# Kernel tuning notes

Hardware: AMD Instinct MI355X
Metric: run time of the kernel (lower is better)

## Reference

```python
import jax, jax.numpy as jnp
import numpy as np

K = 3        # kernel_size
STRIDE = 1
PAD = 1
DIL = 1


def setup_inputs() -> dict:
    key = jax.random.key(0)
    ks = jax.random.split(key, 5)
    B, C, H, W, O = 4, 64, 128, 128, 64
    x = jax.random.normal(ks[0], (B, C, H, W), jnp.float32)
    # small offset-conv weights -> offsets of a few pixels (realistic trained regime)
    offset_w = jax.random.normal(ks[1], (2 * K * K, C, K, K), jnp.float32) * 0.01
    offset_b = jax.random.normal(ks[2], (2 * K * K,), jnp.float32) * 0.01
    weight = jax.random.normal(ks[3], (O, C, K, K), jnp.float32)
    bias = jax.random.normal(ks[4], (O,), jnp.float32)
    return {"x": x, "offset_w": offset_w, "offset_b": offset_b,
            "weight": weight, "bias": bias}


def _conv2d(x, w, b):
    y = jax.lax.conv_general_dilated(
        x, w, window_strides=(STRIDE, STRIDE),
        padding=[(PAD, PAD), (PAD, PAD)],
        dimension_numbers=("NCHW", "OIHW", "NCHW"))
    return y + b[None, :, None, None]


def _deform_conv2d(x, offset, weight, bias):
    B, C, H, W = x.shape
    O = weight.shape[0]
    KK = K * K
    Ho, Wo = offset.shape[2], offset.shape[3]
    # offset channels ordered (y, x) per kernel tap: [B, KK, 2, Ho, Wo]
    off = offset.reshape(B, KK, 2, Ho, Wo)
    kyy, kxx = jnp.meshgrid(jnp.arange(K) * DIL, jnp.arange(K) * DIL, indexing="ij")
    kyy = kyy.reshape(KK).astype(x.dtype)
    kxx = kxx.reshape(KK).astype(x.dtype)
    base_y = (jnp.arange(Ho) * STRIDE - PAD).astype(x.dtype)
    base_x = (jnp.arange(Wo) * STRIDE - PAD).astype(x.dtype)
    # sampling positions [B, KK, Ho, Wo]
    py = base_y[None, None, :, None] + kyy[None, :, None, None] + off[:, :, 0]
    px = base_x[None, None, None, :] + kxx[None, :, None, None] + off[:, :, 1]

    y0 = jnp.floor(py); x0 = jnp.floor(px)
    y1 = y0 + 1.0;      x1 = x0 + 1.0
    wy1 = py - y0; wy0 = 1.0 - wy1
    wx1 = px - x0; wx0 = 1.0 - wx1

    xf = x.reshape(B, C, H * W)

    def corner(yc, xc):
        valid = (yc >= 0) & (yc < H) & (xc >= 0) & (xc < W)  # zero padding outside
        idx = (jnp.clip(yc, 0, H - 1) * W + jnp.clip(xc, 0, W - 1)).astype(jnp.int32)
        g = jax.vmap(lambda xb, ib: xb[:, ib.reshape(-1)])(xf, idx)  # [B, C, KK*Ho*Wo]
        g = g.reshape(B, C, KK, Ho, Wo)
        return g * valid[:, None].astype(x.dtype)

    val = (corner(y0, x0) * (wy0 * wx0)[:, None]
         + corner(y0, x1) * (wy0 * wx1)[:, None]
         + corner(y1, x0) * (wy1 * wx0)[:, None]
         + corner(y1, x1) * (wy1 * wx1)[:, None])  # [B, C, KK, Ho, Wo]

    out = jnp.einsum("bckhw,ock->bohw", val, weight.reshape(O, C, KK))
    return out + bias[None, :, None, None]


def reference(x, offset_w, offset_b, weight, bias):
    offset = _conv2d(x, offset_w, offset_b)
    return _deform_conv2d(x, offset, weight, bias)
```

## Files before the change

### kernel.cpp

```cpp
#include <hip/hip_runtime.h>

#define B_   4
#define C_   64
#define O_   64
#define H_   128
#define W_   128
#define HW_  (H_ * W_)
#define KK_  9
#define M_   18

typedef short  short8  __attribute__((ext_vector_type(8)));
typedef float  floatx4 __attribute__((ext_vector_type(4)));
typedef unsigned short ushort4v __attribute__((ext_vector_type(4)));
typedef unsigned short ushort8v __attribute__((ext_vector_type(8)));

static __device__ __forceinline__ unsigned short f2bf(float f) {
    unsigned int u = __float_as_uint(f);
    u += 0x7FFFu + ((u >> 16) & 1u);
    return (unsigned short)(u >> 16);
}
static __device__ __forceinline__ float bf2f(unsigned short s) {
    return __uint_as_float((unsigned int)s << 16);
}

__global__ __launch_bounds__(256) void prep(
        const float* __restrict__ x, const float* __restrict__ w,
        const float* __restrict__ ow, unsigned short* __restrict__ xT,
        unsigned short* __restrict__ wtbf, unsigned short* __restrict__ owtbf) {
    const int blk = blockIdx.x;
    if (blk < 512) {
        __shared__ unsigned short T[128][72];
        const int tid = threadIdx.x;
        const int y = blk & (H_ - 1);
        const int b = blk >> 7;
        const float* xby = x + (size_t)b * C_ * HW_ + y * W_;
        for (int i = tid; i < C_ * W_; i += 256) {
            const int c = i >> 7, xc = i & 127;
            T[xc][c] = f2bf(xby[(size_t)c * HW_ + xc]);
        }
        __syncthreads();
        unsigned short* dst = xT + (size_t)b * (4 * HW_ * 16) + y * (W_ * 16);
        for (int j = tid; j < 2048; j += 256) {
            const int g  = j >> 9;
            const int x8 = (j >> 2) & 127;
            const int c0 = (j & 3) * 4;
            const ushort4v pk = *(const ushort4v*)&T[x8][g * 16 + c0];
            *(ushort4v*)&dst[(size_t)g * (HW_ * 16) + x8 * 16 + c0] = pk;
        }
    } else if (blk < 530) {
        const int i = (blk - 512) * 256 + threadIdx.x;
        const int lane = i & 63, rest = i >> 6;
        const int ot = rest & 3, cks = rest >> 2;
        const int chunk = cks / 6, ks = cks % 6;
        const int o = ot * 16 + (lane & 15);
        const int kbase = chunk * 192 + ks * 32 + (lane >> 4) * 8;
        ushort8v pk;
        #pragma unroll
        for (int j = 0; j < 8; ++j) {
            const int k = kbase + j;
            pk[j] = f2bf(w[o * 576 + (k & 63) * 9 + (k >> 6)]);
        }
        *(ushort8v*)&wtbf[(size_t)i * 8] = pk;
    } else {
        const int i = (blk - 530) * 256 + threadIdx.x;
        const int lane = i & 63, rest = i >> 6;
        const int tile = rest & 1, tks = rest >> 1;
        const int tap = tks >> 1, ks = tks & 1;
        const int m = tile * 16 + (lane & 15);
        const int cb = ks * 32 + (lane >> 4) * 8;
        ushort8v pk;
        #pragma unroll
        for (int j = 0; j < 8; ++j)
            pk[j] = (m < M_) ? f2bf(ow[m * 576 + (cb + j) * 9 + tap])
                             : (unsigned short)0;
        *(ushort8v*)&owtbf[(size_t)i * 8] = pk;
    }
}

__global__ __launch_bounds__(256, 4) void dcn_fused(
        const unsigned short* __restrict__ xT,
        const unsigned short* __restrict__ owtbf, const float* __restrict__ ob,
        const unsigned short* __restrict__ wtbf, const float* __restrict__ bias,
        float* __restrict__ out) {
    __shared__ union {
        unsigned short P[3][66][72];
        float ep[4][64][17];
    } u;
    __shared__ float offs[4][M_][16];

    const int tid    = threadIdx.x;
    const int lane   = tid & 63;
    const int wslot  = __builtin_amdgcn_readfirstlane(tid >> 6);
    const int lane15 = lane & 15;
    const int quad   = lane >> 4;

    const int g    = blockIdx.x;
    const int xcd  = g & 7;
    const int slot = g >> 3;
    const int ho   = xcd * 16 + (slot >> 3);
    const int b    = (slot >> 1) & 3;
    const int wo_base = (slot & 1) << 6;

    const unsigned short* xTb = xT + (size_t)b * (4 * HW_ * 16);

    #pragma unroll
    for (int it = 0; it < 3; ++it) {
        const int t  = it * 4 + wslot;
        const int ky = t >> 2, cgp = t & 3;
        const int y  = ho - 1 + ky;
        const bool yv = (unsigned)y < (unsigned)H_;
        const unsigned short* src = xTb + (size_t)cgp * (HW_ * 16) + y * (W_ * 16);
        #pragma unroll
        for (int pass = 0; pass < 2; ++pass) {
            const int r = pass * 64 + lane;
            if (r < 66) {
                const int cx = wo_base + r - 1;
                ushort8v p0 = {0, 0, 0, 0, 0, 0, 0, 0};
                ushort8v p1 = {0, 0, 0, 0, 0, 0, 0, 0};
                if (yv && (unsigned)cx < (unsigned)W_) {
                    p0 = *(const ushort8v*)&src[cx * 16];
                    p1 = *(const ushort8v*)&src[cx * 16 + 8];
                }
                *(ushort8v*)&u.P[ky][r][cgp * 16]     = p0;
                *(ushort8v*)&u.P[ky][r][cgp * 16 + 8] = p1;
            }
        }
    }
    __syncthreads();

    floatx4 oa0 = (floatx4){0.f, 0.f, 0.f, 0.f};
    floatx4 oa1 = (floatx4){0.f, 0.f, 0.f, 0.f};
    {
        const int pxt = wslot;
        #pragma unroll
        for (int ky = 0; ky < 3; ++ky) {
            #pragma unroll
            for (int kx = 0; kx < 3; ++kx) {
                const int tap = ky * 3 + kx;
                #pragma unroll
                for (int ks = 0; ks < 2; ++ks) {
                    const int kk = ks * 32 + quad * 8;
                    const short8 af =
                        *(const short8*)&u.P[ky][pxt * 16 + lane15 + kx][kk];
                    const int fb = ((tap * 2 + ks) * 2) * 64 + lane;
                    const short8 bf0 = *(const short8*)&owtbf[(size_t)fb * 8];
                    const short8 bf1 =
                        *(const short8*)&owtbf[(size_t)(fb + 64) * 8];
                    oa0 = __builtin_amdgcn_mfma_f32_16x16x32_bf16(af, bf0, oa0, 0, 0, 0);
                    oa1 = __builtin_amdgcn_mfma_f32_16x16x32_bf16(af, bf1, oa1, 0, 0, 0);
                }
            }
        }
    }
    {
        const float ob0 = ob[lane15];
        #pragma unroll
        for (int r = 0; r < 4; ++r) oa0[r] += ob0;
        *(floatx4*)&offs[wslot][lane15][quad * 4] = oa0;
        if (lane15 < 2) {
            const float ob1 = ob[16 + lane15];
            #pragma unroll
            for (int r = 0; r < 4; ++r) oa1[r] += ob1;
            *(floatx4*)&offs[wslot][16 + lane15][quad * 4] = oa1;
        }
    }
    __syncthreads();

    const int p   = wslot;
    const int pxg = p * 16 + lane15;
    floatx4 acc[4];
    #pragma unroll
    for (int t = 0; t < 4; ++t) acc[t] = (floatx4){0.f, 0.f, 0.f, 0.f};

    for (int chunk = 0; chunk < 3; ++chunk) {
        #pragma unroll
        for (int tl = 0; tl < 3; ++tl) {
            const int k  = chunk * 3 + tl;
            const int ky = k / 3, kx = k % 3;
            const float offy = offs[wslot][2 * k][lane15];
            const float offx = offs[wslot][2 * k + 1][lane15];
            const float py  = (float)(ho - 1 + ky) + offy;
            const float pxx = (float)(wo_base - 1 + kx + pxg) + offx;
            const float fy = floorf(py), fx = floorf(pxx);
            const int y0 = (int)fy, x0 = (int)fx;
            const int y1 = y0 + 1,  x1 = x0 + 1;
            const float wy1 = py - fy,  wy0 = 1.f - wy1;
            const float wx1 = pxx - fx, wx0 = 1.f - wx1;
            const bool y0v = (unsigned)y0 < (unsigned)H_;
            const bool y1v = (unsigned)y1 < (unsigned)H_;
            const bool x0v = (unsigned)x0 < (unsigned)W_;
            const bool x1v = (unsigned)x1 < (unsigned)W_;
            const float w00 = (y0v && x0v) ? wy0 * wx0 : 0.f;
            const float w01 = (y0v && x1v) ? wy0 * wx1 : 0.f;
            const float w10 = (y1v && x0v) ? wy1 * wx0 : 0.f;
            const float w11 = (y1v && x1v) ? wy1 * wx1 : 0.f;
            const int ry0 = min(max(y0, 0), H_ - 1);
            const int ry1 = min(max(y1, 0), H_ - 1);
            const int cx0 = min(max(x0, 0), W_ - 1);
            const int cx1 = min(max(x1, 0), W_ - 1);
            const int a00 = (ry0 * W_ + cx0) * 16;
            const int a01 = (ry0 * W_ + cx1) * 16;
            const int a10 = (ry1 * W_ + cx0) * 16;
            const int a11 = (ry1 * W_ + cx1) * 16;
            #pragma unroll
            for (int chalf = 0; chalf < 2; ++chalf) {
                const int c0 = chalf * 32 + quad * 8;
                const unsigned short* xp =
                    xTb + (size_t)(c0 >> 4) * (HW_ * 16) + (c0 & 8);
                const ushort8v q00 = *(const ushort8v*)&xp[a00];
                const ushort8v q01 = *(const ushort8v*)&xp[a01];
                const ushort8v q10 = *(const ushort8v*)&xp[a10];
                const ushort8v q11 = *(const ushort8v*)&xp[a11];
                ushort8v pk;
                #pragma unroll
                for (int j = 0; j < 8; ++j)
                    pk[j] = f2bf(bf2f(q00[j]) * w00 + bf2f(q01[j]) * w01
                               + bf2f(q10[j]) * w10 + bf2f(q11[j]) * w11);
                const short8 af = *(const short8*)&pk;
                const int cks = chunk * 6 + tl * 2 + chalf;
                #pragma unroll
                for (int t = 0; t < 4; ++t) {
                    const short8 bfrag = *(const short8*)
                        &wtbf[(size_t)((cks * 4 + t) * 64 + lane) * 8];
                    acc[t] = __builtin_amdgcn_mfma_f32_16x16x32_bf16(
                                 af, bfrag, acc[t], 0, 0, 0);
                }
            }
        }
    }

    float* epw = &u.ep[wslot][0][0];
    #pragma unroll
    for (int t = 0; t < 4; ++t)
        #pragma unroll
        for (int r = 0; r < 4; ++r)
            epw[(t * 16 + lane15) * 17 + quad * 4 + r] = acc[t][r];

    const int wo = wo_base + p * 16 + lane15;
    #pragma unroll
    for (int i = 0; i < 16; ++i) {
        const int o = i * 4 + quad;
        out[(size_t)(b * O_ + o) * HW_ + ho * W_ + wo] =
            epw[o * 17 + lane15] + bias[o];
    }
}

extern "C" void kernel_launch(void* const* d_in, const int* in_sizes, int n_in,
                              void* d_out, int out_size, void* d_ws, size_t ws_size,
                              hipStream_t stream) {
    const float* x    = (const float*)d_in[0];
    const float* ow   = (const float*)d_in[1];
    const float* ob   = (const float*)d_in[2];
    const float* w    = (const float*)d_in[3];
    const float* bias = (const float*)d_in[4];
    float* out = (float*)d_out;

    unsigned short* wtbf  = (unsigned short*)d_ws;
    unsigned short* owtbf = wtbf + 4608 * 8;
    unsigned short* xT    = owtbf + 2304 * 8;

    prep<<<539, 256, 0, stream>>>(x, w, ow, xT, wtbf, owtbf);
    dcn_fused<<<B_ * H_ * (W_ / 64), 256, 0, stream>>>(xT, owtbf, ob, wtbf, bias, out);
}
```

Measured before the change: 110.7 us.

## Switch to single-wave 32-pixel blocks using 32x32x16 MFMA

Restructures the fused deformable conv kernel so that each block is a single 64-thread wavefront covering 32 output pixels. Both the offset conv and the main GEMM now use 32x32x16 bf16 MFMAs, and the weight prep layouts are repacked to match. The shared-memory input staging tile and the __syncthreads barriers are removed; the offset conv reads xT directly from global memory. This reduces LDS traffic and synchronization and doubles the number of blocks, at the cost of more global loads for the offset conv and less intra-block reuse.

```diff
diff --git a/kernel.cpp b/kernel.cpp
--- a/kernel.cpp
+++ b/kernel.cpp
@@ -9,8 +9,8 @@
 #define KK_  9
 #define M_   18
 
-typedef short  short8  __attribute__((ext_vector_type(8)));
-typedef float  floatx4 __attribute__((ext_vector_type(4)));
+typedef short  short8   __attribute__((ext_vector_type(8)));
+typedef float  floatx16 __attribute__((ext_vector_type(16)));
 typedef unsigned short ushort4v __attribute__((ext_vector_type(4)));
 typedef unsigned short ushort8v __attribute__((ext_vector_type(8)));
 
@@ -22,6 +22,8 @@
 static __device__ __forceinline__ float bf2f(unsigned short s) {
     return __uint_as_float((unsigned int)s << 16);
 }
+
+#define ZERO16 {0.f,0.f,0.f,0.f,0.f,0.f,0.f,0.f,0.f,0.f,0.f,0.f,0.f,0.f,0.f,0.f}
 
 __global__ __launch_bounds__(256) void prep(
         const float* __restrict__ x, const float* __restrict__ w,
@@ -50,24 +52,22 @@
     } else if (blk < 530) {
         const int i = (blk - 512) * 256 + threadIdx.x;
         const int lane = i & 63, rest = i >> 6;
-        const int ot = rest & 3, cks = rest >> 2;
-        const int chunk = cks / 6, ks = cks % 6;
-        const int o = ot * 16 + (lane & 15);
-        const int kbase = chunk * 192 + ks * 32 + (lane >> 4) * 8;
+        const int t = rest & 1, s = rest >> 1;
+        const int o  = t * 32 + (lane & 31);
+        const int kb = s * 16 + (lane >> 5) * 8;
         ushort8v pk;
         #pragma unroll
         for (int j = 0; j < 8; ++j) {
-            const int k = kbase + j;
+            const int k = kb + j;
             pk[j] = f2bf(w[o * 576 + (k & 63) * 9 + (k >> 6)]);
         }
         *(ushort8v*)&wtbf[(size_t)i * 8] = pk;
     } else {
         const int i = (blk - 530) * 256 + threadIdx.x;
-        const int lane = i & 63, rest = i >> 6;
-        const int tile = rest & 1, tks = rest >> 1;
-        const int tap = tks >> 1, ks = tks & 1;
-        const int m = tile * 16 + (lane & 15);
-        const int cb = ks * 32 + (lane >> 4) * 8;
+        const int lane = i & 63, s = i >> 6;
+        const int m   = lane & 31;
+        const int tap = s >> 2;
+        const int cb  = (s & 3) * 16 + (lane >> 5) * 8;
         ushort8v pk;
         #pragma unroll
         for (int j = 0; j < 8; ++j)
@@ -77,171 +77,121 @@
     }
 }
 
-__global__ __launch_bounds__(256, 4) void dcn_fused(
+__global__ __launch_bounds__(64, 4) void dcn_fused(
         const unsigned short* __restrict__ xT,
         const unsigned short* __restrict__ owtbf, const float* __restrict__ ob,
         const unsigned short* __restrict__ wtbf, const float* __restrict__ bias,
         float* __restrict__ out) {
-    __shared__ union {
-        unsigned short P[3][66][72];
-        float ep[4][64][17];
-    } u;
-    __shared__ float offs[4][M_][16];
-
-    const int tid    = threadIdx.x;
-    const int lane   = tid & 63;
-    const int wslot  = __builtin_amdgcn_readfirstlane(tid >> 6);
-    const int lane15 = lane & 15;
-    const int quad   = lane >> 4;
+    __shared__ float offs[M_][33];
+    __shared__ float epw[64][33];
+
+    const int lane = threadIdx.x;
+    const int pxl  = lane & 31;
+    const int kh   = lane >> 5;
+    const int khOff = kh * 8;
 
     const int g    = blockIdx.x;
     const int xcd  = g & 7;
     const int slot = g >> 3;
-    const int ho   = xcd * 16 + (slot >> 3);
-    const int b    = (slot >> 1) & 3;
-    const int wo_base = (slot & 1) << 6;
+    const int ho   = xcd * 16 + (slot >> 4);
+    const int rest = slot & 15;
+    const int b    = rest >> 2;
+    const int wo_base = (rest & 3) << 5;
 
     const unsigned short* xTb = xT + (size_t)b * (4 * HW_ * 16);
 
+    floatx16 oa = ZERO16;
+    for (int tap = 0; tap < 9; ++tap) {
+        const int ky = tap / 3, kx = tap % 3;
+        const int y    = ho - 1 + ky;
+        const int xcol = wo_base - 1 + kx + pxl;
+        const bool valid = ((unsigned)y < (unsigned)H_) &&
+                           ((unsigned)xcol < (unsigned)W_);
+        const int yc = min(max(y, 0), H_ - 1);
+        const int xc = min(max(xcol, 0), W_ - 1);
+        const int base = (yc * W_ + xc) * 16 + khOff;
+        #pragma unroll
+        for (int sl = 0; sl < 4; ++sl) {
+            ushort8v q = {0, 0, 0, 0, 0, 0, 0, 0};
+            if (valid)
+                q = *(const ushort8v*)&xTb[(size_t)sl * (HW_ * 16) + base];
+            const short8 af = *(const short8*)&q;
+            const int s = tap * 4 + sl;
+            const short8 bf = *(const short8*)&owtbf[(size_t)(s * 64 + lane) * 8];
+            oa = __builtin_amdgcn_mfma_f32_32x32x16_bf16(af, bf, oa, 0, 0, 0);
+        }
+    }
+    if (pxl < M_) {
+        const float obm = ob[pxl];
+        #pragma unroll
+        for (int r = 0; r < 16; ++r) {
+            const int px = (r & 3) + 8 * (r >> 2) + 4 * kh;
+            offs[pxl][px] = oa[r] + obm;
+        }
+    }
+
+    floatx16 acc0 = ZERO16, acc1 = ZERO16;
+    for (int tap = 0; tap < 9; ++tap) {
+        const int ky = tap / 3, kx = tap % 3;
+        const float offy = offs[2 * tap][pxl];
+        const float offx = offs[2 * tap + 1][pxl];
+        const float py  = (float)(ho - 1 + ky) + offy;
+        const float pxx = (float)(wo_base - 1 + kx + pxl) + offx;
+        const float fy = floorf(py), fx = floorf(pxx);
+        const int y0 = (int)fy, x0 = (int)fx;
+        const int y1 = y0 + 1,  x1 = x0 + 1;
+        const float wy1 = py - fy,  wy0 = 1.f - wy1;
+        const float wx1 = pxx - fx, wx0 = 1.f - wx1;
+        const bool y0v = (unsigned)y0 < (unsigned)H_;
+        const bool y1v = (unsigned)y1 < (unsigned)H_;
+        const bool x0v = (unsigned)x0 < (unsigned)W_;
+        const bool x1v = (unsigned)x1 < (unsigned)W_;
+        const float w00 = (y0v && x0v) ? wy0 * wx0 : 0.f;
+        const float w01 = (y0v && x1v) ? wy0 * wx1 : 0.f;
+        const float w10 = (y1v && x0v) ? wy1 * wx0 : 0.f;
+        const float w11 = (y1v && x1v) ? wy1 * wx1 : 0.f;
+        const int ry0 = min(max(y0, 0), H_ - 1);
+        const int ry1 = min(max(y1, 0), H_ - 1);
+        const int cx0 = min(max(x0, 0), W_ - 1);
+        const int cx1 = min(max(x1, 0), W_ - 1);
+        const int a00 = (ry0 * W_ + cx0) * 16 + khOff;
+        const int a01 = (ry0 * W_ + cx1) * 16 + khOff;
+        const int a10 = (ry1 * W_ + cx0) * 16 + khOff;
+        const int a11 = (ry1 * W_ + cx1) * 16 + khOff;
+        #pragma unroll
+        for (int sl = 0; sl < 4; ++sl) {
+            const unsigned short* xp = xTb + (size_t)sl * (HW_ * 16);
+            const ushort8v q00 = *(const ushort8v*)&xp[a00];
+            const ushort8v q01 = *(const ushort8v*)&xp[a01];
+            const ushort8v q10 = *(const ushort8v*)&xp[a10];
+            const ushort8v q11 = *(const ushort8v*)&xp[a11];
+            ushort8v pk;
+            #pragma unroll
+            for (int j = 0; j < 8; ++j)
+                pk[j] = f2bf(bf2f(q00[j]) * w00 + bf2f(q01[j]) * w01
+                           + bf2f(q10[j]) * w10 + bf2f(q11[j]) * w11);
+            const short8 af = *(const short8*)&pk;
+            const int s = tap * 4 + sl;
+            const short8 bf0 = *(const short8*)
+                &wtbf[(size_t)((s * 2 + 0) * 64 + lane) * 8];
+            const short8 bf1 = *(const short8*)
+                &wtbf[(size_t)((s * 2 + 1) * 64 + lane) * 8];
+            acc0 = __builtin_amdgcn_mfma_f32_32x32x16_bf16(af, bf0, acc0, 0, 0, 0);
+            acc1 = __builtin_amdgcn_mfma_f32_32x32x16_bf16(af, bf1, acc1, 0, 0, 0);
+        }
+    }
+
     #pragma unroll
-    for (int it = 0; it < 3; ++it) {
-        const int t  = it * 4 + wslot;
-        const int ky = t >> 2, cgp = t & 3;
-        const int y  = ho - 1 + ky;
-        const bool yv = (unsigned)y < (unsigned)H_;
-        const unsigned short* src = xTb + (size_t)cgp * (HW_ * 16) + y * (W_ * 16);
-        #pragma unroll
-        for (int pass = 0; pass < 2; ++pass) {
-            const int r = pass * 64 + lane;
-            if (r < 66) {
-                const int cx = wo_base + r - 1;
-                ushort8v p0 = {0, 0, 0, 0, 0, 0, 0, 0};
-                ushort8v p1 = {0, 0, 0, 0, 0, 0, 0, 0};
-                if (yv && (unsigned)cx < (unsigned)W_) {
-                    p0 = *(const ushort8v*)&src[cx * 16];
-                    p1 = *(const ushort8v*)&src[cx * 16 + 8];
-                }
-                *(ushort8v*)&u.P[ky][r][cgp * 16]     = p0;
-                *(ushort8v*)&u.P[ky][r][cgp * 16 + 8] = p1;
-            }
-        }
-    }
-    __syncthreads();
-
-    floatx4 oa0 = (floatx4){0.f, 0.f, 0.f, 0.f};
-    floatx4 oa1 = (floatx4){0.f, 0.f, 0.f, 0.f};
-    {
-        const int pxt = wslot;
-        #pragma unroll
-        for (int ky = 0; ky < 3; ++ky) {
-            #pragma unroll
-            for (int kx = 0; kx < 3; ++kx) {
-                const int tap = ky * 3 + kx;
-                #pragma unroll
-                for (int ks = 0; ks < 2; ++ks) {
-                    const int kk = ks * 32 + quad * 8;
-                    const short8 af =
-                        *(const short8*)&u.P[ky][pxt * 16 + lane15 + kx][kk];
-                    const int fb = ((tap * 2 + ks) * 2) * 64 + lane;
-                    const short8 bf0 = *(const short8*)&owtbf[(size_t)fb * 8];
-                    const short8 bf1 =
-                        *(const short8*)&owtbf[(size_t)(fb + 64) * 8];
-                    oa0 = __builtin_amdgcn_mfma_f32_16x16x32_bf16(af, bf0, oa0, 0, 0, 0);
-                    oa1 = __builtin_amdgcn_mfma_f32_16x16x32_bf16(af, bf1, oa1, 0, 0, 0);
-                }
-            }
-        }
-    }
-    {
-        const float ob0 = ob[lane15];
-        #pragma unroll
-        for (int r = 0; r < 4; ++r) oa0[r] += ob0;
-        *(floatx4*)&offs[wslot][lane15][quad * 4] = oa0;
-        if (lane15 < 2) {
-            const float ob1 = ob[16 + lane15];
-            #pragma unroll
-            for (int r = 0; r < 4; ++r) oa1[r] += ob1;
-            *(floatx4*)&offs[wslot][16 + lane15][quad * 4] = oa1;
-        }
-    }
-    __syncthreads();
-
-    const int p   = wslot;
-    const int pxg = p * 16 + lane15;
-    floatx4 acc[4];
+    for (int r = 0; r < 16; ++r) {
+        const int px = (r & 3) + 8 * (r >> 2) + 4 * kh;
+        epw[pxl][px]      = acc0[r];
+        epw[32 + pxl][px] = acc1[r];
+    }
+    const size_t obase = (size_t)b * O_ * HW_ + ho * W_ + wo_base;
     #pragma unroll
-    for (int t = 0; t < 4; ++t) acc[t] = (floatx4){0.f, 0.f, 0.f, 0.f};
-
-    for (int chunk = 0; chunk < 3; ++chunk) {
-        #pragma unroll
-        for (int tl = 0; tl < 3; ++tl) {
-            const int k  = chunk * 3 + tl;
-            const int ky = k / 3, kx = k % 3;
-            const float offy = offs[wslot][2 * k][lane15];
-            const float offx = offs[wslot][2 * k + 1][lane15];
-            const float py  = (float)(ho - 1 + ky) + offy;
-            const float pxx = (float)(wo_base - 1 + kx + pxg) + offx;
-            const float fy = floorf(py), fx = floorf(pxx);
-            const int y0 = (int)fy, x0 = (int)fx;
-            const int y1 = y0 + 1,  x1 = x0 + 1;
-            const float wy1 = py - fy,  wy0 = 1.f - wy1;
-            const float wx1 = pxx - fx, wx0 = 1.f - wx1;
-            const bool y0v = (unsigned)y0 < (unsigned)H_;
-            const bool y1v = (unsigned)y1 < (unsigned)H_;
-            const bool x0v = (unsigned)x0 < (unsigned)W_;
-            const bool x1v = (unsigned)x1 < (unsigned)W_;
-            const float w00 = (y0v && x0v) ? wy0 * wx0 : 0.f;
-            const float w01 = (y0v && x1v) ? wy0 * wx1 : 0.f;
-            const float w10 = (y1v && x0v) ? wy1 * wx0 : 0.f;
-            const float w11 = (y1v && x1v) ? wy1 * wx1 : 0.f;
-            const int ry0 = min(max(y0, 0), H_ - 1);
-            const int ry1 = min(max(y1, 0), H_ - 1);
-            const int cx0 = min(max(x0, 0), W_ - 1);
-            const int cx1 = min(max(x1, 0), W_ - 1);
-            const int a00 = (ry0 * W_ + cx0) * 16;
-            const int a01 = (ry0 * W_ + cx1) * 16;
-            const int a10 = (ry1 * W_ + cx0) * 16;
-            const int a11 = (ry1 * W_ + cx1) * 16;
-            #pragma unroll
-            for (int chalf = 0; chalf < 2; ++chalf) {
-                const int c0 = chalf * 32 + quad * 8;
-                const unsigned short* xp =
-                    xTb + (size_t)(c0 >> 4) * (HW_ * 16) + (c0 & 8);
-                const ushort8v q00 = *(const ushort8v*)&xp[a00];
-                const ushort8v q01 = *(const ushort8v*)&xp[a01];
-                const ushort8v q10 = *(const ushort8v*)&xp[a10];
-                const ushort8v q11 = *(const ushort8v*)&xp[a11];
-                ushort8v pk;
-                #pragma unroll
-                for (int j = 0; j < 8; ++j)
-                    pk[j] = f2bf(bf2f(q00[j]) * w00 + bf2f(q01[j]) * w01
-                               + bf2f(q10[j]) * w10 + bf2f(q11[j]) * w11);
-                const short8 af = *(const short8*)&pk;
-                const int cks = chunk * 6 + tl * 2 + chalf;
-                #pragma unroll
-                for (int t = 0; t < 4; ++t) {
-                    const short8 bfrag = *(const short8*)
-                        &wtbf[(size_t)((cks * 4 + t) * 64 + lane) * 8];
-                    acc[t] = __builtin_amdgcn_mfma_f32_16x16x32_bf16(
-                                 af, bfrag, acc[t], 0, 0, 0);
-                }
-            }
-        }
-    }
-
-    float* epw = &u.ep[wslot][0][0];
-    #pragma unroll
-    for (int t = 0; t < 4; ++t)
-        #pragma unroll
-        for (int r = 0; r < 4; ++r)
-            epw[(t * 16 + lane15) * 17 + quad * 4 + r] = acc[t][r];
-
-    const int wo = wo_base + p * 16 + lane15;
-    #pragma unroll
-    for (int i = 0; i < 16; ++i) {
-        const int o = i * 4 + quad;
-        out[(size_t)(b * O_ + o) * HW_ + ho * W_ + wo] =
-            epw[o * 17 + lane15] + bias[o];
+    for (int i = 0; i < 32; ++i) {
+        const int o = i * 2 + kh;
+        out[obase + (size_t)o * HW_ + pxl] = epw[o][pxl] + bias[o];
     }
 }
 
@@ -260,5 +210,5 @@
     unsigned short* xT    = owtbf + 2304 * 8;
 
     prep<<<539, 256, 0, stream>>>(x, w, ow, xT, wtbf, owtbf);
-    dcn_fused<<<B_ * H_ * (W_ / 64), 256, 0, stream>>>(xT, owtbf, ob, wtbf, bias, out);
-}
+    dcn_fused<<<B_ * H_ * (W_ / 32), 64, 0, stream>>>(xT, owtbf, ob, wtbf, bias, out);
+}
```

New measurement: 129.1 us. 1.17x slower.
